# Performance work log

Measured on AMD Instinct MI355X. Metric: run time of the kernel, lower is better.

The kernel has to match this reference:

```python
import jax, jax.numpy as jnp
import numpy as np

B, S, D, H = 2, 2048, 1024, 16
DH = D // H  # key_dim = embed_dim // num_heads
NEG = 1e9    # Keras masked-softmax adder magnitude
EPS = 1e-6


def setup_inputs() -> dict:
    key = jax.random.key(0)
    ks = jax.random.split(key, 6)
    sc = 1.0 / np.sqrt(D)
    return {
        "x": jax.random.normal(ks[0], (B, S, D), jnp.float32),
        "Wq": jax.random.normal(ks[1], (D, H, DH), jnp.float32) * sc,
        "bq": jnp.zeros((H, DH), jnp.float32),
        "Wk": jax.random.normal(ks[2], (D, H, DH), jnp.float32) * sc,
        "bk": jnp.zeros((H, DH), jnp.float32),
        "Wv": jax.random.normal(ks[3], (D, H, DH), jnp.float32) * sc,
        "bv": jnp.zeros((H, DH), jnp.float32),
        "Wo": jax.random.normal(ks[4], (H, DH, D), jnp.float32) * (1.0 / np.sqrt(D)),
        "bo": jnp.zeros((D,), jnp.float32),
        "gamma": jnp.ones((D,), jnp.float32),
        "beta": jnp.zeros((D,), jnp.float32),
    }


def reference(x, Wq, bq, Wk, bk, Wv, bv, Wo, bo, gamma, beta):
    # Keras MultiHeadAttention(query=x, value=x), inference (dropouts are identity)
    q = jnp.einsum("bsd,dhk->bshk", x, Wq) + bq  # [B,S,H,DH]
    k = jnp.einsum("bsd,dhk->bshk", x, Wk) + bk
    v = jnp.einsum("bsd,dhk->bshk", x, Wv) + bv

    scores = jnp.einsum("bqhd,bkhd->bhqk", q, k) / jnp.sqrt(jnp.asarray(DH, x.dtype))
    # Source: mask = 1 - band_part(ones, -1, 0) -> ones strictly ABOVE diagonal.
    # Keras attends where mask==1 and adds (1-mask)*(-1e9) elsewhere. Faithful:
    i = jnp.arange(S)[:, None]
    j = jnp.arange(S)[None, :]
    allowed = (j > i).astype(scores.dtype)  # [S,S], strict upper triangle
    scores = scores + (allowed - 1.0) * NEG  # subtract 1e9 where not allowed
    probs = jax.nn.softmax(scores, axis=-1)

    ctx = jnp.einsum("bhqk,bkhd->bqhd", probs, v)  # [B,S,H,DH]
    attn_out = jnp.einsum("bqhd,hdo->bqo", ctx, Wo) + bo  # [B,S,D]

    # residual + LayerNorm(eps=1e-6)
    y = x + attn_out
    mu = jnp.mean(y, axis=-1, keepdims=True)
    var = jnp.mean(jnp.square(y - mu), axis=-1, keepdims=True)
    return (y - mu) * jax.lax.rsqrt(var + EPS) * gamma + beta
```

## Files before the change

### kernel.cpp

```cpp
#include <hip/hip_runtime.h>
#include <hip/hip_bf16.h>

typedef __hip_bfloat16 bf16;
typedef __attribute__((ext_vector_type(8))) short bf16x8;
typedef __attribute__((ext_vector_type(4))) float f32x4;

constexpr int Bc  = 2;
constexpr int Sc  = 2048;
constexpr int Dc  = 1024;
constexpr int Hc  = 16;
constexpr int DHc = 64;
constexpr int BS  = Bc * Sc;
constexpr int NT  = Sc / 64;

__device__ __forceinline__ float bs2f(unsigned short u) {
    union { unsigned int i; float f; } v; v.i = ((unsigned int)u) << 16; return v.f;
}
__device__ __forceinline__ short f2bs(float x) {
    bf16 h = __float2bfloat16(x);
    return *reinterpret_cast<short*>(&h);
}

typedef const __attribute__((address_space(1))) unsigned int* as1_u32p;
typedef __attribute__((address_space(3))) unsigned int* as3_u32p;
__device__ __forceinline__ void gl_lds16(const void* g, void* l) {
    __builtin_amdgcn_global_load_lds((as1_u32p)g, (as3_u32p)l, 16, 0, 0);
}

__global__ __launch_bounds__(256) void prep(
    const float* __restrict__ x, short* __restrict__ xb,
    const float* __restrict__ w0, const float* __restrict__ w1,
    const float* __restrict__ w2, const float* __restrict__ w3,
    short* __restrict__ WT)
{
    __shared__ float T[64][65];
    const int i = blockIdx.x;
    const int t = threadIdx.x;

    if (i < 4096) {
        const int off = i * 1024 + t * 4;
        const float4 v = *(const float4*)(x + off);
        ushort4 o;
        o.x = (unsigned short)f2bs(v.x);
        o.y = (unsigned short)f2bs(v.y);
        o.z = (unsigned short)f2bs(v.z);
        o.w = (unsigned short)f2bs(v.w);
        *(ushort4*)(xb + off) = o;
        return;
    }

    const int idx = i - 4096;
    const int z  = idx >> 8;
    const int k0 = (idx & 15) * 64;
    const int n0 = ((idx >> 4) & 15) * 64;
    const float* in = (z == 0) ? w0 : (z == 1) ? w1 : (z == 2) ? w2 : w3;
    short* out = WT + (size_t)z * 1024 * 1024;
    #pragma unroll
    for (int it = 0; it < 4; ++it) {
        const int s = it * 256 + t;
        const int r = s >> 4, c = (s & 15) * 4;
        *(float4*)&T[r][c] = *(const float4*)(in + (size_t)(k0 + r) * 1024 + n0 + c);
    }
    __syncthreads();
    #pragma unroll
    for (int it = 0; it < 4; ++it) {
        const int s = it * 256 + t;
        const int rr = s >> 4, cc = (s & 15) * 4;
        ushort4 o;
        o.x = (unsigned short)f2bs(T[cc + 0][rr]);
        o.y = (unsigned short)f2bs(T[cc + 1][rr]);
        o.z = (unsigned short)f2bs(T[cc + 2][rr]);
        o.w = (unsigned short)f2bs(T[cc + 3][rr]);
        *(ushort4*)(out + (size_t)(n0 + rr) * 1024 + k0 + cc) = o;
    }
}

__global__ __launch_bounds__(256, 3) void gemm_bt(
    const short* __restrict__ A, const short* __restrict__ BTbase,
    const float* __restrict__ b0, const float* __restrict__ b1,
    const float* __restrict__ b2, short* __restrict__ Cbase,
    const float sc0)
{
    __shared__ __align__(16) short As[128 * 64];
    __shared__ __align__(16) short Bs[128 * 64];

    const int z = blockIdx.z;
    const short* BT = BTbase + (size_t)z * 1024 * 1024;
    const float* bias = (z == 0) ? b0 : (z == 1) ? b1 : b2;
    const float sc = (z == 0) ? sc0 : 1.0f;
    short* C = Cbase + (size_t)z * BS * Dc;

    const int t = threadIdx.x;
    const int lane = t & 63, w = t >> 6;
    const int quad = lane >> 4, l16 = lane & 15;
    const int wm = (w & 1) * 64, wn = (w >> 1) * 64;
    const int row0 = blockIdx.y * 128;
    const int col0 = blockIdx.x * 128;
    const int sw = l16 & 7;

    f32x4 acc[4][4] = {};

    for (int kt = 0; kt < 1024; kt += 64) {
        __syncthreads();
        #pragma unroll
        for (int i = 0; i < 4; ++i) {
            const int f = i * 256 + t;
            const int r = f >> 3;
            const int g = (f & 7) ^ (r & 7);
            short* lb = &As[(i * 256 + w * 64) * 8];
            gl_lds16(A + (size_t)(row0 + r) * 1024 + kt + g * 8, lb);
            short* lb2 = &Bs[(i * 256 + w * 64) * 8];
            gl_lds16(BT + (size_t)(col0 + r) * 1024 + kt + g * 8, lb2);
        }
        __syncthreads();
        #pragma unroll
        for (int ks = 0; ks < 2; ++ks) {
            bf16x8 av[4], bv[4];
            #pragma unroll
            for (int mt = 0; mt < 4; ++mt) {
                const int r = wm + mt * 16 + l16;
                av[mt] = *(const bf16x8*)&As[r * 64 + ((ks * 4 + quad) ^ sw) * 8];
            }
            #pragma unroll
            for (int nt = 0; nt < 4; ++nt) {
                const int r = wn + nt * 16 + l16;
                bv[nt] = *(const bf16x8*)&Bs[r * 64 + ((ks * 4 + quad) ^ sw) * 8];
            }
            #pragma unroll
            for (int mt = 0; mt < 4; ++mt)
                #pragma unroll
                for (int nt = 0; nt < 4; ++nt)
                    acc[mt][nt] = __builtin_amdgcn_mfma_f32_16x16x32_bf16(
                        av[mt], bv[nt], acc[mt][nt], 0, 0, 0);
        }
    }

    float bvv[4];
    #pragma unroll
    for (int nt = 0; nt < 4; ++nt) bvv[nt] = bias[col0 + wn + nt * 16 + l16];
    #pragma unroll
    for (int mt = 0; mt < 4; ++mt)
        #pragma unroll
        for (int reg = 0; reg < 4; ++reg) {
            const size_t row = row0 + wm + mt * 16 + quad * 4 + reg;
            #pragma unroll
            for (int nt = 0; nt < 4; ++nt) {
                const int col = col0 + wn + nt * 16 + l16;
                C[row * 1024 + col] = f2bs((acc[mt][nt][reg] + bvv[nt]) * sc);
            }
        }
}

__global__ __launch_bounds__(256, 3) void gemm_bt_n64(
    const short* __restrict__ A, const short* __restrict__ BT,
    const float* __restrict__ bias, short* __restrict__ C)
{
    __shared__ __align__(16) short As[128 * 64];
    __shared__ __align__(16) short Bs[64 * 64];

    const int t = threadIdx.x;
    const int lane = t & 63, w = t >> 6;
    const int quad = lane >> 4, l16 = lane & 15;
    const int wm = (w & 1) * 64, wn = (w >> 1) * 32;
    const int row0 = blockIdx.y * 128;
    const int col0 = blockIdx.x * 64;
    const int sw = l16 & 7;

    f32x4 acc[4][2] = {};

    for (int kt = 0; kt < 1024; kt += 64) {
        __syncthreads();
        #pragma unroll
        for (int i = 0; i < 4; ++i) {
            const int f = i * 256 + t;
            const int r = f >> 3;
            const int g = (f & 7) ^ (r & 7);
            gl_lds16(A + (size_t)(row0 + r) * 1024 + kt + g * 8,
                     &As[(i * 256 + w * 64) * 8]);
        }
        #pragma unroll
        for (int i = 0; i < 2; ++i) {
            const int f = i * 256 + t;
            const int r = f >> 3;
            const int g = (f & 7) ^ (r & 7);
            gl_lds16(BT + (size_t)(col0 + r) * 1024 + kt + g * 8,
                     &Bs[(i * 256 + w * 64) * 8]);
        }
        __syncthreads();
        #pragma unroll
        for (int ks = 0; ks < 2; ++ks) {
            bf16x8 av[4], bv[2];
            #pragma unroll
            for (int mt = 0; mt < 4; ++mt) {
                const int r = wm + mt * 16 + l16;
                av[mt] = *(const bf16x8*)&As[r * 64 + ((ks * 4 + quad) ^ sw) * 8];
            }
            #pragma unroll
            for (int nt = 0; nt < 2; ++nt) {
                const int r = wn + nt * 16 + l16;
                bv[nt] = *(const bf16x8*)&Bs[r * 64 + ((ks * 4 + quad) ^ sw) * 8];
            }
            #pragma unroll
            for (int mt = 0; mt < 4; ++mt)
                #pragma unroll
                for (int nt = 0; nt < 2; ++nt)
                    acc[mt][nt] = __builtin_amdgcn_mfma_f32_16x16x32_bf16(
                        av[mt], bv[nt], acc[mt][nt], 0, 0, 0);
        }
    }

    float bvv[2];
    #pragma unroll
    for (int nt = 0; nt < 2; ++nt) bvv[nt] = bias[col0 + wn + nt * 16 + l16];
    #pragma unroll
    for (int mt = 0; mt < 4; ++mt)
        #pragma unroll
        for (int reg = 0; reg < 4; ++reg) {
            const size_t row = row0 + wm + mt * 16 + quad * 4 + reg;
            #pragma unroll
            for (int nt = 0; nt < 2; ++nt) {
                const int col = col0 + wn + nt * 16 + l16;
                C[row * 1024 + col] = f2bs(acc[mt][reg == reg ? nt : nt][reg] + bvv[nt]);
            }
        }
}

__global__ __launch_bounds__(256, 3) void attn_mfma(
    const short* __restrict__ Qg, const short* __restrict__ Kg,
    const short* __restrict__ Vg, short* __restrict__ CTX)
{
    __shared__ __align__(16) short VsT[2][64][72];
    __shared__ __align__(16) short Ps[4][16][72];
    __shared__ float red[4][64];

    const int tid  = threadIdx.x;

    if (blockIdx.y == 16) {
        const int h = blockIdx.x, b = blockIdx.z;
        const int dh = tid & 63, ck = tid >> 6;
        float s = 0.f;
        const short* vp = Vg + ((size_t)b * Sc + ck * 512) * Dc + h * DHc + dh;
        for (int j = 0; j < 512; ++j) s += bs2f(vp[(size_t)j * Dc]);
        red[ck][dh] = s;
        __syncthreads();
        if (ck == 0) {
            const float tot = (red[0][dh] + red[1][dh] + red[2][dh] + red[3][dh]) * (1.f / Sc);
            CTX[((size_t)b * Sc + Sc - 1) * Dc + h * DHc + dh] = f2bs(tot);
        }
        return;
    }

    const int lane = tid & 63, w = tid >> 6;
    const int quad = lane >> 4, l16 = lane & 15;

    const int xcd   = blockIdx.x & 7;
    const int local = (blockIdx.x >> 3) + 2 * blockIdx.y + 32 * blockIdx.z;
    const int bh    = xcd * 4 + (local >> 4);
    const int p     = local & 15;
    const int h     = bh & 15;
    const int b     = bh >> 4;
    const size_t rb = (size_t)b * Sc;
    const int cb = h * DHc;

    const int skey = tid & 63, sseg = (tid >> 6) * 8;
    const int pkey = ((skey & 15) << 2) | (skey >> 4);

    bf16x8 ones;
    #pragma unroll
    for (int e = 0; e < 8; ++e) ones[e] = (short)0x3F80;

    const size_t tstride = (size_t)64 * Dc;

    #pragma unroll 1
    for (int ph = 0; ph < 2; ++ph) {
        const int myq = ph ? (NT - 1 - p) : p;
        const int t0  = myq;
        const int q0  = myq * 64;

        bf16x8 qf[2];
        {
            const short* qp = Qg + (rb + q0 + w * 16 + l16) * (size_t)Dc + cb + quad * 8;
            qf[0] = *(const bf16x8*)(qp);
            qf[1] = *(const bf16x8*)(qp + 32);
        }
        f32x4 lacc = {};
        f32x4 O[4] = {};

        const short* kfp = Kg + (rb + (size_t)t0 * 64 + l16) * Dc + cb + quad * 8;
        const short* vp = Vg + (rb + (size_t)t0 * 64 + skey) * Dc + cb + sseg;

        bf16x8 kf[2][4];
        #pragma unroll
        for (int ks = 0; ks < 2; ++ks)
            #pragma unroll
            for (int nt = 0; nt < 4; ++nt)
                kf[ks][nt] = *(const bf16x8*)(kfp + (size_t)nt * 16 * Dc + ks * 32);

        if (ph) __syncthreads();

        {
            const int buf = t0 & 1;
            const bf16x8 v0v = *(const bf16x8*)(vp);
            const bf16x8 v1v = *(const bf16x8*)(vp + 32);
            #pragma unroll
            for (int e = 0; e < 8; ++e) {
                VsT[buf][sseg + e][pkey]      = v0v[e];
                VsT[buf][sseg + 32 + e][pkey] = v1v[e];
            }
        }
        __syncthreads();

        for (int t = t0; t < NT; ++t) {
            const int cur = t & 1;
            const bool havenext = (t + 1 < NT);
            bf16x8 pv0, pv1;
            if (havenext) {
                pv0 = *(const bf16x8*)(vp + tstride);
                pv1 = *(const bf16x8*)(vp + tstride + 32);
            }

            f32x4 S[4] = {};
            __builtin_amdgcn_s_setprio(1);
            #pragma unroll
            for (int ks = 0; ks < 2; ++ks)
                #pragma unroll
                for (int nt = 0; nt < 4; ++nt)
                    S[nt] = __builtin_amdgcn_mfma_f32_16x16x32_bf16(
                        qf[ks], kf[ks][nt], S[nt], 0, 0, 0);
            __builtin_amdgcn_s_setprio(0);

            if (havenext) {
                const short* kp_ = kfp + tstride;
                #pragma unroll
                for (int ks = 0; ks < 2; ++ks)
                    #pragma unroll
                    for (int nt = 0; nt < 4; ++nt)
                        kf[ks][nt] = *(const bf16x8*)(kp_ + (size_t)nt * 16 * Dc + ks * 32);
            }

            #pragma unroll
            for (int nt = 0; nt < 4; ++nt) {
                #pragma unroll
                for (int reg = 0; reg < 4; ++reg) {
                    float s = fminf(S[nt][reg], 115.4f);
                    if (t == t0) {
                        const int col = t * 64 + nt * 16 + l16;
                        const int row = q0 + w * 16 + quad * 4 + reg;
                        s = (col > row) ? s : -126.0f;
                    }
                    S[nt][reg] = exp2f(s);
                }
            }

            #pragma unroll
            for (int reg = 0; reg < 4; ++reg) {
                const __hip_bfloat162 lo = __float22bfloat162_rn(make_float2(S[0][reg], S[1][reg]));
                const __hip_bfloat162 hi = __float22bfloat162_rn(make_float2(S[2][reg], S[3][reg]));
                uint2 u;
                u.x = *reinterpret_cast<const unsigned int*>(&lo);
                u.y = *reinterpret_cast<const unsigned int*>(&hi);
                *(uint2*)&Ps[w][quad * 4 + reg][l16 * 4] = u;
            }

            __builtin_amdgcn_s_setprio(1);
            #pragma unroll
            for (int ks = 0; ks < 2; ++ks) {
                const bf16x8 pf = *(const bf16x8*)&Ps[w][l16][ks * 32 + quad * 8];
                lacc = __builtin_amdgcn_mfma_f32_16x16x32_bf16(pf, ones, lacc, 0, 0, 0);
                #pragma unroll
                for (int nt = 0; nt < 4; ++nt) {
                    const bf16x8 vf = *(const bf16x8*)&VsT[cur][nt * 16 + l16][ks * 32 + quad * 8];
                    O[nt] = __builtin_amdgcn_mfma_f32_16x16x32_bf16(pf, vf, O[nt], 0, 0, 0);
                }
            }
            __builtin_amdgcn_s_setprio(0);

            if (havenext) {
                const int nb = cur ^ 1;
                #pragma unroll
                for (int e = 0; e < 8; ++e) {
                    VsT[nb][sseg + e][pkey]      = pv0[e];
                    VsT[nb][sseg + 32 + e][pkey] = pv1[e];
                }
                __syncthreads();
            }
            kfp += tstride;
            vp  += tstride;
        }

        float inv[4];
        #pragma unroll
        for (int reg = 0; reg < 4; ++reg) inv[reg] = 1.0f / lacc[reg];
        #pragma unroll
        for (int nt = 0; nt < 4; ++nt)
            #pragma unroll
            for (int reg = 0; reg < 4; ++reg) {
                const int lr = q0 + w * 16 + quad * 4 + reg;
                if (lr != Sc - 1)
                    CTX[(rb + lr) * Dc + cb + nt * 16 + l16] = f2bs(O[nt][reg] * inv[reg]);
            }
    }
}

__global__ __launch_bounds__(256, 4) void resid_ln(
    const float* __restrict__ X, const short* __restrict__ AO,
    const float* __restrict__ gamma, const float* __restrict__ beta,
    float* __restrict__ out)
{
    const int r = blockIdx.x;
    const int t = threadIdx.x;
    const size_t base = (size_t)r * Dc + t * 4;

    const float4 x4 = *(const float4*)(X + base);
    const ushort4 a4 = *(const ushort4*)(AO + base);
    float y[4];
    y[0] = x4.x + bs2f(a4.x);
    y[1] = x4.y + bs2f(a4.y);
    y[2] = x4.z + bs2f(a4.z);
    y[3] = x4.w + bs2f(a4.w);

    float s  = y[0] + y[1] + y[2] + y[3];
    float s2 = y[0]*y[0] + y[1]*y[1] + y[2]*y[2] + y[3]*y[3];
    #pragma unroll
    for (int off = 1; off < 64; off <<= 1) {
        s  += __shfl_xor(s,  off, 64);
        s2 += __shfl_xor(s2, off, 64);
    }
    __shared__ float red[8];
    const int w = t >> 6;
    if ((t & 63) == 0) { red[w] = s; red[4 + w] = s2; }
    __syncthreads();
    s  = red[0] + red[1] + red[2] + red[3];
    s2 = red[4] + red[5] + red[6] + red[7];

    const float mu   = s * (1.0f / Dc);
    const float rstd = rsqrtf(s2 * (1.0f / Dc) - mu * mu + 1e-6f);

    const float4 g4 = *(const float4*)(gamma + t * 4);
    const float4 b4 = *(const float4*)(beta  + t * 4);
    float4 o;
    o.x = (y[0] - mu) * rstd * g4.x + b4.x;
    o.y = (y[1] - mu) * rstd * g4.y + b4.y;
    o.z = (y[2] - mu) * rstd * g4.z + b4.z;
    o.w = (y[3] - mu) * rstd * g4.w + b4.w;
    *(float4*)(out + base) = o;
}

extern "C" void kernel_launch(void* const* d_in, const int* in_sizes, int n_in,
                              void* d_out, int out_size, void* d_ws, size_t ws_size,
                              hipStream_t stream)
{
    (void)in_sizes; (void)n_in; (void)out_size; (void)ws_size;
    const float* x     = (const float*)d_in[0];
    const float* Wq    = (const float*)d_in[1];
    const float* bq    = (const float*)d_in[2];
    const float* Wk    = (const float*)d_in[3];
    const float* bk    = (const float*)d_in[4];
    const float* Wv    = (const float*)d_in[5];
    const float* bv    = (const float*)d_in[6];
    const float* Wo    = (const float*)d_in[7];
    const float* bo    = (const float*)d_in[8];
    const float* gamma = (const float*)d_in[9];
    const float* beta  = (const float*)d_in[10];
    float* out = (float*)d_out;

    const size_t matN = (size_t)BS * Dc;
    const size_t wN   = (size_t)Dc * Dc;
    short* xb = (short*)d_ws;
    short* WT = xb + matN;
    short* Qb = WT + 4 * wN;
    short* Kb = Qb + matN;
    short* Vb = Kb + matN;
    short* Cx = Vb + matN;
    short* AO = Qb;

    prep<<<5120, 256, 0, stream>>>(x, xb, Wq, Wk, Wv, Wo, WT);

    dim3 gq(Dc / 128, BS / 128, 3);
    gemm_bt<<<gq, 256, 0, stream>>>(xb, WT, bq, bk, bv, Qb, 0.18033688f);

    dim3 ga(16, 17, 2);
    attn_mfma<<<ga, 256, 0, stream>>>(Qb, Kb, Vb, Cx);

    dim3 go(Dc / 64, BS / 128, 1);
    gemm_bt_n64<<<go, 256, 0, stream>>>(Cx, WT + 3 * wN, bo, AO);

    resid_ln<<<BS, 256, 0, stream>>>(x, AO, gamma, beta, out);
}
```

Measured before the change: 226.7 us.

## Stage K tiles through double-buffered shared memory and template the diagonal step

Before this change each wave loaded its own full K fragments from global memory every tile, so the 4 waves of a block fetched the same K tile four times. K now gets the same cooperative, double-buffered LDS staging as V: each thread loads one slice, and the MFMA operands are read back from LDS. The per-tile body moves into a templated helper, so the causal-mask branch is resolved at compile time and only the diagonal tile pays for masking. This adds about 18 KB of LDS per block, which may reduce occupancy, and adds LDS read traffic.

```diff
diff --git a/kernel.cpp b/kernel.cpp
--- a/kernel.cpp
+++ b/kernel.cpp
@@ -220,15 +220,81 @@
             #pragma unroll
             for (int nt = 0; nt < 2; ++nt) {
                 const int col = col0 + wn + nt * 16 + l16;
-                C[row * 1024 + col] = f2bs(acc[mt][reg == reg ? nt : nt][reg] + bvv[nt]);
-            }
-        }
+                C[row * 1024 + col] = f2bs(acc[mt][nt][reg] + bvv[nt]);
+            }
+        }
+}
+
+
+template<bool DIAG>
+__device__ __forceinline__ void qtile_step(
+    const bf16x8 (&qf)[2],
+    const short (&Ks)[64][72], const short (&VsT)[64][72],
+    short (&Psw)[16][72],
+    const int k0, const int row_base,
+    const int quad, const int l16,
+    const bf16x8 ones,
+    f32x4 &lacc, f32x4 (&O)[4])
+{
+    bf16x8 kf[2][4];
+    #pragma unroll
+    for (int ks = 0; ks < 2; ++ks)
+        #pragma unroll
+        for (int nt = 0; nt < 4; ++nt)
+            kf[ks][nt] = *(const bf16x8*)&Ks[nt * 16 + l16][ks * 32 + quad * 8];
+
+    f32x4 S[4] = {};
+    __builtin_amdgcn_s_setprio(1);
+    #pragma unroll
+    for (int ks = 0; ks < 2; ++ks)
+        #pragma unroll
+        for (int nt = 0; nt < 4; ++nt)
+            S[nt] = __builtin_amdgcn_mfma_f32_16x16x32_bf16(qf[ks], kf[ks][nt], S[nt], 0, 0, 0);
+    __builtin_amdgcn_s_setprio(0);
+
+    #pragma unroll
+    for (int nt = 0; nt < 4; ++nt) {
+        #pragma unroll
+        for (int reg = 0; reg < 4; ++reg) {
+            float s = fminf(S[nt][reg], 115.4f);
+            if (DIAG) {
+                const int col = k0 + nt * 16 + l16;
+                const int row = row_base + quad * 4 + reg;
+                s = (col > row) ? s : -126.0f;
+            }
+            S[nt][reg] = exp2f(s);
+        }
+    }
+
+    #pragma unroll
+    for (int reg = 0; reg < 4; ++reg) {
+        const __hip_bfloat162 lo = __float22bfloat162_rn(make_float2(S[0][reg], S[1][reg]));
+        const __hip_bfloat162 hi = __float22bfloat162_rn(make_float2(S[2][reg], S[3][reg]));
+        uint2 u;
+        u.x = *reinterpret_cast<const unsigned int*>(&lo);
+        u.y = *reinterpret_cast<const unsigned int*>(&hi);
+        *(uint2*)&Psw[quad * 4 + reg][l16 * 4] = u;
+    }
+
+    __builtin_amdgcn_s_setprio(1);
+    #pragma unroll
+    for (int ks = 0; ks < 2; ++ks) {
+        const bf16x8 pf = *(const bf16x8*)&Psw[l16][ks * 32 + quad * 8];
+        lacc = __builtin_amdgcn_mfma_f32_16x16x32_bf16(pf, ones, lacc, 0, 0, 0);
+        #pragma unroll
+        for (int nt = 0; nt < 4; ++nt) {
+            const bf16x8 vf = *(const bf16x8*)&VsT[nt * 16 + l16][ks * 32 + quad * 8];
+            O[nt] = __builtin_amdgcn_mfma_f32_16x16x32_bf16(pf, vf, O[nt], 0, 0, 0);
+        }
+    }
+    __builtin_amdgcn_s_setprio(0);
 }
 
 __global__ __launch_bounds__(256, 3) void attn_mfma(
     const short* __restrict__ Qg, const short* __restrict__ Kg,
     const short* __restrict__ Vg, short* __restrict__ CTX)
 {
+    __shared__ __align__(16) short Ks [2][64][72];
     __shared__ __align__(16) short VsT[2][64][72];
     __shared__ __align__(16) short Ps[4][16][72];
     __shared__ float red[4][64];
@@ -286,22 +352,19 @@
         f32x4 lacc = {};
         f32x4 O[4] = {};
 
-        const short* kfp = Kg + (rb + (size_t)t0 * 64 + l16) * Dc + cb + quad * 8;
+        const short* kp = Kg + (rb + (size_t)t0 * 64 + skey) * Dc + cb + sseg;
         const short* vp = Vg + (rb + (size_t)t0 * 64 + skey) * Dc + cb + sseg;
-
-        bf16x8 kf[2][4];
-        #pragma unroll
-        for (int ks = 0; ks < 2; ++ks)
-            #pragma unroll
-            for (int nt = 0; nt < 4; ++nt)
-                kf[ks][nt] = *(const bf16x8*)(kfp + (size_t)nt * 16 * Dc + ks * 32);
 
         if (ph) __syncthreads();
 
         {
             const int buf = t0 & 1;
+            const bf16x8 k0v = *(const bf16x8*)(kp);
+            const bf16x8 k1v = *(const bf16x8*)(kp + 32);
             const bf16x8 v0v = *(const bf16x8*)(vp);
             const bf16x8 v1v = *(const bf16x8*)(vp + 32);
+            *(bf16x8*)&Ks[buf][skey][sseg]      = k0v;
+            *(bf16x8*)&Ks[buf][skey][sseg + 32] = k1v;
             #pragma unroll
             for (int e = 0; e < 8; ++e) {
                 VsT[buf][sseg + e][pkey]      = v0v[e];
@@ -313,70 +376,25 @@
         for (int t = t0; t < NT; ++t) {
             const int cur = t & 1;
             const bool havenext = (t + 1 < NT);
-            bf16x8 pv0, pv1;
+            bf16x8 pk0, pk1, pv0, pv1;
             if (havenext) {
+                pk0 = *(const bf16x8*)(kp + tstride);
+                pk1 = *(const bf16x8*)(kp + tstride + 32);
                 pv0 = *(const bf16x8*)(vp + tstride);
                 pv1 = *(const bf16x8*)(vp + tstride + 32);
             }
 
-            f32x4 S[4] = {};
-            __builtin_amdgcn_s_setprio(1);
-            #pragma unroll
-            for (int ks = 0; ks < 2; ++ks)
-                #pragma unroll
-                for (int nt = 0; nt < 4; ++nt)
-                    S[nt] = __builtin_amdgcn_mfma_f32_16x16x32_bf16(
-                        qf[ks], kf[ks][nt], S[nt], 0, 0, 0);
-            __builtin_amdgcn_s_setprio(0);
-
-            if (havenext) {
-                const short* kp_ = kfp + tstride;
-                #pragma unroll
-                for (int ks = 0; ks < 2; ++ks)
-                    #pragma unroll
-                    for (int nt = 0; nt < 4; ++nt)
-                        kf[ks][nt] = *(const bf16x8*)(kp_ + (size_t)nt * 16 * Dc + ks * 32);
-            }
-
-            #pragma unroll
-            for (int nt = 0; nt < 4; ++nt) {
-                #pragma unroll
-                for (int reg = 0; reg < 4; ++reg) {
-                    float s = fminf(S[nt][reg], 115.4f);
-                    if (t == t0) {
-                        const int col = t * 64 + nt * 16 + l16;
-                        const int row = q0 + w * 16 + quad * 4 + reg;
-                        s = (col > row) ? s : -126.0f;
-                    }
-                    S[nt][reg] = exp2f(s);
-                }
-            }
-
-            #pragma unroll
-            for (int reg = 0; reg < 4; ++reg) {
-                const __hip_bfloat162 lo = __float22bfloat162_rn(make_float2(S[0][reg], S[1][reg]));
-                const __hip_bfloat162 hi = __float22bfloat162_rn(make_float2(S[2][reg], S[3][reg]));
-                uint2 u;
-                u.x = *reinterpret_cast<const unsigned int*>(&lo);
-                u.y = *reinterpret_cast<const unsigned int*>(&hi);
-                *(uint2*)&Ps[w][quad * 4 + reg][l16 * 4] = u;
-            }
-
-            __builtin_amdgcn_s_setprio(1);
-            #pragma unroll
-            for (int ks = 0; ks < 2; ++ks) {
-                const bf16x8 pf = *(const bf16x8*)&Ps[w][l16][ks * 32 + quad * 8];
-                lacc = __builtin_amdgcn_mfma_f32_16x16x32_bf16(pf, ones, lacc, 0, 0, 0);
-                #pragma unroll
-                for (int nt = 0; nt < 4; ++nt) {
-                    const bf16x8 vf = *(const bf16x8*)&VsT[cur][nt * 16 + l16][ks * 32 + quad * 8];
-                    O[nt] = __builtin_amdgcn_mfma_f32_16x16x32_bf16(pf, vf, O[nt], 0, 0, 0);
-                }
-            }
-            __builtin_amdgcn_s_setprio(0);
+            if (t == t0)
+                qtile_step<true >(qf, Ks[cur], VsT[cur], Ps[w],
+                                  t * 64, q0 + w * 16, quad, l16, ones, lacc, O);
+            else
+                qtile_step<false>(qf, Ks[cur], VsT[cur], Ps[w],
+                                  t * 64, q0 + w * 16, quad, l16, ones, lacc, O);
 
             if (havenext) {
                 const int nb = cur ^ 1;
+                *(bf16x8*)&Ks[nb][skey][sseg]      = pk0;
+                *(bf16x8*)&Ks[nb][skey][sseg + 32] = pk1;
                 #pragma unroll
                 for (int e = 0; e < 8; ++e) {
                     VsT[nb][sseg + e][pkey]      = pv0[e];
@@ -384,8 +402,8 @@
                 }
                 __syncthreads();
             }
-            kfp += tstride;
-            vp  += tstride;
+            kp += tstride;
+            vp += tstride;
         }
 
         float inv[4];
```

New measurement: 195.1 us. 1.16x faster.
